# Optimization experiments

Hardware: AMD Instinct MI355X
Metric: run time of the kernel (lower is better)

## Reference

```python
import jax, jax.numpy as jnp
import numpy as np

B, S, F, H, T = 1024, 64, 2, 128, 24  # batch, src_len, n_features, hidden, output_length


def setup_inputs() -> dict:
    key = jax.random.key(0)
    ks = jax.random.split(key, 20)
    def p(k, shape):
        return jax.random.normal(k, shape, jnp.float32) * 0.05
    return {
        "x": jax.random.normal(ks[0], (B, S, F), jnp.float32),
        "prev_y": jnp.zeros((B, F), jnp.float32),
        # encoder 3-layer LSTM (PyTorch gate order i,f,g,o; b = b_ih + b_hh fused)
        "enc_Wih0": p(ks[1], (4 * H, F)),
        "enc_Whh0": p(ks[2], (4 * H, H)),
        "enc_b0": p(ks[3], (4 * H,)),
        "enc_Wih12": p(ks[4], (2, 4 * H, H)),
        "enc_Whh12": p(ks[5], (2, 4 * H, H)),
        "enc_b12": p(ks[6], (2, 4 * H)),
        # Bahdanau attention
        "attn_W": p(ks[7], (H, 2 * H)),
        "attn_b": p(ks[8], (H,)),
        "v_W": p(ks[9], (H,)),
        # decoder 3-layer LSTM, input size H+2
        "dec_Wih0": p(ks[10], (4 * H, H + 2)),
        "dec_Whh0": p(ks[11], (4 * H, H)),
        "dec_b0": p(ks[12], (4 * H,)),
        "dec_Wih12": p(ks[13], (2, 4 * H, H)),
        "dec_Whh12": p(ks[14], (2, 4 * H, H)),
        "dec_b12": p(ks[15], (2, 4 * H)),
        # output head Linear(2H, 2)
        "out_W": p(ks[16], (2, 2 * H)),
        "out_b": p(ks[17], (2,)),
    }


def _lstm_cell(xt, h, c, Wih, Whh, b):
    g = xt @ Wih.T + h @ Whh.T + b  # [B, 4H]
    i, f, gg, o = jnp.split(g, 4, axis=-1)
    c = jax.nn.sigmoid(f) * c + jax.nn.sigmoid(i) * jnp.tanh(gg)
    h = jax.nn.sigmoid(o) * jnp.tanh(c)
    return h, c


def _lstm_layer(xs, Wih, Whh, b):
    # xs: [S, B, in] -> hs [S, B, H], final (h, c)
    z = jnp.zeros((xs.shape[1], Whh.shape[1]), xs.dtype)
    def step(carry, xt):
        h, c = _lstm_cell(xt, carry[0], carry[1], Wih, Whh, b)
        return (h, c), h
    (hT, cT), hs = jax.lax.scan(step, (z, z), xs)
    return hs, hT, cT


def reference(x, prev_y, enc_Wih0, enc_Whh0, enc_b0, enc_Wih12, enc_Whh12, enc_b12,
              attn_W, attn_b, v_W, dec_Wih0, dec_Whh0, dec_b0, dec_Wih12, dec_Whh12,
              dec_b12, out_W, out_b):
    # ---- encoder: 3-layer LSTM over time ----
    hs, h0, c0 = _lstm_layer(jnp.swapaxes(x, 0, 1), enc_Wih0, enc_Whh0, enc_b0)
    hid, cel = [h0], [c0]
    for l in range(2):
        hs, hT, cT = _lstm_layer(hs, enc_Wih12[l], enc_Whh12[l], enc_b12[l])
        hid.append(hT); cel.append(cT)
    enc_out = jnp.swapaxes(hs, 0, 1)            # [B, S, H]
    h = jnp.stack(hid)                           # [3, B, H]
    c = jnp.stack(cel)

    def dec_step(carry, _):
        prev_out, h, c = carry
        h_top = h[2]                                             # top-layer hidden [B, H]
        a_in = jnp.concatenate(
            [jnp.broadcast_to(h_top[:, None, :], enc_out.shape), enc_out], axis=-1)  # [B, S, 2H]
        scores = jnp.tanh(a_in @ attn_W.T + attn_b) @ v_W        # [B, S]
        attw = jax.nn.softmax(scores, axis=1)
        weighted = jnp.einsum('bs,bsd->bd', attw, enc_out)        # [B, H]
        rnn_in = jnp.concatenate([prev_out, weighted], axis=-1)   # [B, H+2]
        h0n, c0n = _lstm_cell(rnn_in, h[0], c[0], dec_Wih0, dec_Whh0, dec_b0)
        h1n, c1n = _lstm_cell(h0n, h[1], c[1], dec_Wih12[0], dec_Whh12[0], dec_b12[0])
        h2n, c2n = _lstm_cell(h1n, h[2], c[2], dec_Wih12[1], dec_Whh12[1], dec_b12[1])
        out = jnp.concatenate([h2n, weighted], axis=-1) @ out_W.T + out_b  # [B, 2]
        return (out, jnp.stack([h0n, h1n, h2n]), jnp.stack([c0n, c1n, c2n])), out

    _, outs = jax.lax.scan(dec_step, (prev_y, h, c), None, length=T)
    return outs  # [T, B, 2]
```

## Files before the change

### kernel.cpp

```cpp
#include <hip/hip_runtime.h>
#include <hip/hip_fp16.h>

#define SEQ   64
#define HID   128
#define TOUT  24

typedef unsigned int u32;
typedef _Float16 f16;
typedef __attribute__((ext_vector_type(8))) f16 f16x8;
typedef __attribute__((ext_vector_type(4))) float f32x4;
#define MFMA __builtin_amdgcn_mfma_f32_16x16x32_f16

static __device__ __forceinline__ float sigm(float x){
  return __builtin_amdgcn_rcpf(1.f + __expf(-x));
}
static __device__ __forceinline__ float tanh_fast(float x){
  return fmaf(2.f, __builtin_amdgcn_rcpf(1.f + __expf(-2.f*x)), -1.f);
}

__global__ void prep_kernel(
    const float* __restrict__ eWih0,  const float* __restrict__ eWhh0,
    const float* __restrict__ eWih12, const float* __restrict__ eWhh12,
    const float* __restrict__ aW,
    const float* __restrict__ dWih0,  const float* __restrict__ dWhh0,
    const float* __restrict__ dWih12, const float* __restrict__ dWhh12,
    const float* __restrict__ oW,
    __half* __restrict__ wE0, __half* __restrict__ wE1, __half* __restrict__ wE2,
    __half* __restrict__ wD0, __half* __restrict__ wD1, __half* __restrict__ wD2,
    __half* __restrict__ wAh, __half* __restrict__ wAeF, float* __restrict__ wOT,
    float* __restrict__ dW2)
{
  int id = blockIdx.x*blockDim.x + threadIdx.x;
  if (id < 65536){
    int m=id, jj=m&7, l=(m>>3)&63, kt=(m>>9)&3, nt=m>>11;
    int col = nt*16 + (l&15), k = kt*32 + ((l>>4)<<3) + jj;
    wE0[m] = __float2half(eWhh0[col*128 + k]); return;
  }
  id -= 65536;
  if (id < 5*131072){
    int seg = id >> 17, m = id & 131071;
    int jj=m&7, l=(m>>3)&63, kt=(m>>9)&7, nt=m>>12;
    int col = nt*16 + (l&15), k = kt*32 + ((l>>4)<<3) + jj;
    float v;
    if (seg==0)      v = (k<128)? eWih12[col*128+k]         : eWhh12[col*128 + (k-128)];
    else if (seg==1) v = (k<128)? eWih12[65536+col*128+k]   : eWhh12[65536 + col*128 + (k-128)];
    else if (seg==2) v = (k<128)? dWih0[col*130 + 2 + k]    : dWhh0[col*128 + (k-128)];
    else if (seg==3) v = (k<128)? dWih12[col*128+k]         : dWhh12[col*128 + (k-128)];
    else             v = (k<128)? dWih12[65536+col*128+k]   : dWhh12[65536 + col*128 + (k-128)];
    __half* dst = (seg==0)?wE1:(seg==1)?wE2:(seg==2)?wD0:(seg==3)?wD1:wD2;
    dst[m] = __float2half(v); return;
  }
  id -= 5*131072;
  if (id < 16384){
    int m=id, jj=m&7, l=(m>>3)&63, kt=(m>>9)&3, nt=m>>11;
    int col = nt*16 + (l&15), k = kt*32 + ((l>>4)<<3) + jj;
    wAh[m] = __float2half(aW[col*256 + k]); return;
  }
  id -= 16384;
  if (id < 16384){
    int m=id, jj=m&7, l=(m>>3)&63, kt=(m>>9)&3, nt=m>>11;
    int col = nt*16 + (l&15), k = kt*32 + ((l>>4)<<3) + jj;
    wAeF[m] = __float2half(aW[col*256 + 128 + k]); return;
  }
  id -= 16384;
  if (id < 512){ int k=id>>1, jo=id&1; wOT[id] = oW[jo*256 + k]; return; }
  id -= 512;
  if (id < 1024){ int col=id>>1, ki=id&1; dW2[id] = dWih0[col*130 + ki]; return; }
}

__global__ __launch_bounds__(512) __attribute__((amdgpu_waves_per_eu(2, 2)))
void enc_kernel(
    const float* __restrict__ x, const float* __restrict__ eb0,
    const float* __restrict__ eb12, const float* __restrict__ eWih0,
    const __half* __restrict__ wE0, const __half* __restrict__ wE1,
    const __half* __restrict__ wE2,
    __half* __restrict__ hs0, __half* __restrict__ hs1,
    __half* __restrict__ carryH, float* __restrict__ carryC)
{
  __shared__ __align__(16) __half hT[2][2048];

  const int tid = threadIdx.x, w = tid>>6, lane = tid&63;
  const int l15 = lane&15, g4 = lane>>4;
  const int j = w*16 + l15;
  const int b16 = blockIdx.x*16;
  const int K0 = ((j>>5)*64 + ((j>>3)&3)*16)*8 + (j&7);

  __half* hs0b = hs0 + (size_t)blockIdx.x*131072;
  __half* hs1b = hs1 + (size_t)blockIdx.x*131072;

  for (int layer=0; layer<3; ++layer){
    const __half* W  = (layer==0)? wE0 : (layer==1)? wE1 : wE2;
    const float* bs  = (layer==0)? eb0 : (layer==1)? eb12 : (eb12+512);
    const __half* hinb  = (layer==1)? hs0b : hs1b;
    __half* houtb = (layer==0)? hs0b : (layer==1)? hs1b : nullptr;

    float bias[4];
#pragma unroll
    for (int g=0; g<4; ++g) bias[g] = bs[g*128 + j];
    float2 wx[4];
    if (layer==0){
#pragma unroll
      for (int g=0; g<4; ++g) wx[g] = *(const float2*)(eWih0 + (g*128+j)*2);
    }
    const f16x8* wb = (const f16x8*)W + lane;
    f16x8 Wh[16];
    if (layer==0){
#pragma unroll
      for (int g=0; g<4; ++g)
#pragma unroll
        for (int kt=0; kt<4; ++kt) Wh[g*4+kt] = wb[(size_t)((g*8+w)*4 + kt)*64];
    } else {
#pragma unroll
      for (int g=0; g<4; ++g)
#pragma unroll
        for (int kt=0; kt<4; ++kt) Wh[g*4+kt] = wb[(size_t)((g*8+w)*8 + 4 + kt)*64];
    }
    float c[4] = {0.f,0.f,0.f,0.f};
    ((u32*)hT[0])[tid] = 0u; ((u32*)hT[0])[tid+512] = 0u;
    __syncthreads();

    float2 xv[4]; f16x8 alo[4];
    if (layer==0){
#pragma unroll
      for (int q=0; q<4; ++q) xv[q] = *(const float2*)(x + ((size_t)(b16+g4*4+q)*SEQ + 0)*2);
    } else {
#pragma unroll
      for (int kt=0; kt<4; ++kt) alo[kt] = *(const f16x8*)(hinb + (kt*64+lane)*8);
    }

    int cur = 0;
    for (int t=0; t<SEQ; ++t){
      f16x8 wi[16];
      if (layer>0){
#pragma unroll
        for (int g=0; g<4; ++g)
#pragma unroll
          for (int kt=0; kt<4; ++kt) wi[g*4+kt] = wb[(size_t)((g*8+w)*8 + kt)*64];
      }
      f16x8 ah[4];
#pragma unroll
      for (int kt=0; kt<4; ++kt) ah[kt] = *(const f16x8*)(hT[cur] + (kt*64+lane)*8);
      float2 xcur[4]; f16x8 acur[4];
      if (layer==0){
#pragma unroll
        for (int q=0; q<4; ++q) xcur[q] = xv[q];
        if (t+1 < SEQ)
#pragma unroll
          for (int q=0; q<4; ++q) xv[q] = *(const float2*)(x + ((size_t)(b16+g4*4+q)*SEQ + t+1)*2);
      } else {
#pragma unroll
        for (int kt=0; kt<4; ++kt) acur[kt] = alo[kt];
        if (t+1 < SEQ)
#pragma unroll
          for (int kt=0; kt<4; ++kt) alo[kt] = *(const f16x8*)(hinb + (size_t)(t+1)*2048 + (kt*64+lane)*8);
      }
      f32x4 acc[4];
#pragma unroll
      for (int g=0; g<4; ++g) acc[g] = (f32x4){0.f,0.f,0.f,0.f};
#pragma unroll
      for (int g=0; g<4; ++g)
#pragma unroll
        for (int kt=0; kt<4; ++kt) acc[g] = MFMA(ah[kt], Wh[g*4+kt], acc[g], 0,0,0);
      if (layer>0){
#pragma unroll
        for (int g=0; g<4; ++g)
#pragma unroll
          for (int kt=0; kt<4; ++kt) acc[g] = MFMA(acur[kt], wi[g*4+kt], acc[g], 0,0,0);
      }
#pragma unroll
      for (int q=0; q<4; ++q){
        float gi = acc[0][q]+bias[0], gf = acc[1][q]+bias[1],
              gg = acc[2][q]+bias[2], go = acc[3][q]+bias[3];
        if (layer==0){
          gi += xcur[q].x*wx[0].x + xcur[q].y*wx[0].y;
          gf += xcur[q].x*wx[1].x + xcur[q].y*wx[1].y;
          gg += xcur[q].x*wx[2].x + xcur[q].y*wx[2].y;
          go += xcur[q].x*wx[3].x + xcur[q].y*wx[3].y;
        }
        float cn = fmaf(sigm(gf), c[q], sigm(gi)*tanh_fast(gg));
        float hn = sigm(go)*tanh_fast(cn);
        c[q] = cn;
        __half hh = __float2half(hn);
        hT[cur^1][K0 + (g4*4+q)*8] = hh;
        if (layer < 2){
          houtb[(size_t)t*2048 + K0 + (g4*4+q)*8] = hh;
        } else {
          int off = g4*32768 + q*8192 + (t>>4)*2048 + (j>>5)*512
                  + ((t&15) + ((j>>3)&3)*16)*8 + (j&7);
          hs0b[off] = hh;
        }
        if (t == SEQ-1){
          int ci = (layer*1024 + b16 + g4*4 + q)*128 + j;
          carryH[ci] = hh;
          carryC[ci] = cn;
        }
      }
      __syncthreads();
      cur ^= 1;
    }
    __syncthreads();
  }
}

#define LDQ(Q, g, kh) \
  Q[0] = wb[(size_t)((g)*64 + (kh)*4 + 0)*64]; \
  Q[1] = wb[(size_t)((g)*64 + (kh)*4 + 1)*64]; \
  Q[2] = wb[(size_t)((g)*64 + (kh)*4 + 2)*64]; \
  Q[3] = wb[(size_t)((g)*64 + (kh)*4 + 3)*64];
#define MM4(Q, A, g) \
  acc[g] = MFMA(A[0], Q[0], acc[g], 0,0,0); \
  acc[g] = MFMA(A[1], Q[1], acc[g], 0,0,0); \
  acc[g] = MFMA(A[2], Q[2], acc[g], 0,0,0); \
  acc[g] = MFMA(A[3], Q[3], acc[g], 0,0,0);

static __device__ __forceinline__ void dec_gemm(const __half* __restrict__ W,
    const __half* __restrict__ A0, const __half* __restrict__ A1,
    f32x4* acc, int lane, int w8)
{
  const f16x8* wb = (const f16x8*)W + (size_t)(w8*8)*64 + lane;
  f16x8 q0[4], q1[4], q2[4], q3[4];
  f16x8 a0[4], a1[4];
  LDQ(q0, 0, 0)
  LDQ(q1, 1, 0)
  LDQ(q2, 2, 0)
#pragma unroll
  for (int kt=0; kt<4; ++kt) a0[kt] = *(const f16x8*)(A0 + (kt*64+lane)*8);
#pragma unroll
  for (int g=0; g<4; ++g) acc[g] = (f32x4){0.f,0.f,0.f,0.f};
  MM4(q0, a0, 0)  LDQ(q3, 3, 0)
  MM4(q1, a0, 1)  LDQ(q0, 0, 1)
#pragma unroll
  for (int kt=0; kt<4; ++kt) a1[kt] = *(const f16x8*)(A1 + (kt*64+lane)*8);
  MM4(q2, a0, 2)  LDQ(q1, 1, 1)
  MM4(q3, a0, 3)  LDQ(q2, 2, 1)
  MM4(q0, a1, 0)  LDQ(q3, 3, 1)
  MM4(q1, a1, 1)
  MM4(q2, a1, 2)
  MM4(q3, a1, 3)
}

__global__ __launch_bounds__(512) __attribute__((amdgpu_waves_per_eu(2, 2)))
void dec_kernel(
    const float* __restrict__ prev_y, const float* __restrict__ db0,
    const float* __restrict__ db12, const float* __restrict__ ob,
    const float* __restrict__ ab, const float* __restrict__ vW,
    const __half* __restrict__ wD0, const __half* __restrict__ wD1,
    const __half* __restrict__ wD2, const __half* __restrict__ wAh,
    const __half* __restrict__ wAeF, const float* __restrict__ wOT,
    const float* __restrict__ dW2, const __half* __restrict__ encAg,
    const __half* __restrict__ carryH, const float* __restrict__ carryC,
    float* __restrict__ dout)
{
  __shared__ __align__(16) __half hT[4][2048];
  __shared__ float hp[4][132];
  __shared__ float scbF[256];
  __shared__ __align__(16) __half scb16h[256];
  __shared__ float hw[4*256];
  __shared__ float po[4][2];
  __shared__ float vwl[128];
  extern __shared__ __align__(16) __half dyn[];
  __half* encBL = dyn;
  __half* epL   = dyn + 32768;

  const int tid = threadIdx.x, w = tid>>6, lane = tid&63;
  const int l15 = lane&15, g4 = lane>>4;
  const int d = blockIdx.x, b4 = d*4;
  const int w8 = (w + d) & 7;
  const int j = w8*16 + l15;
  const int K0 = ((j>>5)*64 + ((j>>3)&3)*16)*8 + (j&7);
  const __half* encAd = encAg + (size_t)(d>>2)*131072 + (size_t)(d&3)*32768;

  float cD[3][4];
  if (g4 == 0){
#pragma unroll
    for (int l=0; l<3; ++l)
#pragma unroll
      for (int q=0; q<4; ++q){
        int ci = (l*1024 + b4 + q)*128 + j;
        hT[1+l][K0 + q*8] = carryH[ci];
        cD[l][q] = carryC[ci];
      }
  }
  if (tid < 8) po[tid>>1][tid&1] = prev_y[(b4 + (tid>>1))*2 + (tid&1)];
  if (tid < 128) vwl[tid] = vW[tid];

#pragma unroll
  for (int it=0; it<8; ++it){
    int lin = it*512 + tid;
    f16x8 v = *(const f16x8*)(encAd + (size_t)lin*8);
    int laneA = lin&63, ktA = (lin>>6)&3, sb = (lin>>8)&3, r4 = (lin>>10)&3;
    int s  = sb*16 + (laneA&15);
    int d0 = ktA*32 + ((laneA>>4)<<3);
    int base = r4*8192 + ((d0>>4)*2 + (s>>5))*512 + (s&7);
    int lb0  = (d0&15) + ((s>>3)&3)*16;
    f16* eb = (f16*)encBL;
#pragma unroll
    for (int u=0; u<8; ++u) eb[base + (lb0+u)*8] = v[u];
  }
#pragma unroll
  for (int i=0; i<2; ++i){
    int mt = w*2 + i, r4 = mt>>2, sb = mt&3;
    f16x8 a[4];
#pragma unroll
    for (int kt=0; kt<4; ++kt)
      a[kt] = *(const f16x8*)(encAd + (size_t)(((r4*4+sb)*4 + kt)*64 + lane)*8);
    const f16x8* bw = (const f16x8*)wAeF + lane;
#pragma unroll
    for (int nt=0; nt<8; ++nt){
      int col = nt*16 + l15;
      float abv = ab[col];
      f32x4 acc = {abv, abv, abv, abv};
#pragma unroll
      for (int kt=0; kt<4; ++kt) acc = MFMA(a[kt], bw[(size_t)(nt*4+kt)*64], acc, 0,0,0);
      int srow = r4*64 + sb*16 + g4*4;
#pragma unroll
      for (int q=0; q<4; ++q) epL[(srow+q)*132 + col] = __float2half(acc[q]);
    }
  }
  __syncthreads();

  auto cell = [&](float* crl, const float* bdp, const float* dwp, __half* hdst, float* hwp,
                  const f32x4* acc){
    float b0 = bdp[j], b1 = bdp[128+j], b2 = bdp[256+j], b3 = bdp[384+j];
    float2 w0, w1, w2, w3;
    if (dwp){
      w0 = *(const float2*)(dwp + 2*j);
      w1 = *(const float2*)(dwp + 2*(128+j));
      w2 = *(const float2*)(dwp + 2*(256+j));
      w3 = *(const float2*)(dwp + 2*(384+j));
    }
#pragma unroll
    for (int q=0; q<4; ++q){
      float gi = acc[0][q]+b0, gf = acc[1][q]+b1, gg = acc[2][q]+b2, go = acc[3][q]+b3;
      if (dwp){
        float p0 = po[q][0], p1 = po[q][1];
        gi += p0*w0.x + p1*w0.y;
        gf += p0*w1.x + p1*w1.y;
        gg += p0*w2.x + p1*w2.y;
        go += p0*w3.x + p1*w3.y;
      }
      float cn = fmaf(sigm(gf), crl[q], sigm(gi)*tanh_fast(gg));
      float hn = sigm(go)*tanh_fast(cn);
      crl[q] = cn;
      hdst[K0 + q*8] = __float2half(hn);
      if (hwp) hwp[q*256 + j] = hn;
    }
  };

  int zr = 0;
  for (int t=0; t<TOUT; ++t){
    asm volatile("" : "+v"(zr));
    const float*  db0t  = db0  + zr;
    const float*  db12t = db12 + zr;
    const float*  dW2t  = dW2  + zr;
    const __half* wAht  = wAh  + zr;

    {
      f16x8 a[4], wAhR[4];
      const f16x8* wbh = (const f16x8*)wAht + lane;
#pragma unroll
      for (int kt=0; kt<4; ++kt) wAhR[kt] = wbh[(size_t)(w8*4+kt)*64];
#pragma unroll
      for (int kt=0; kt<4; ++kt) a[kt] = *(const f16x8*)(hT[3] + (kt*64+lane)*8);
      f32x4 acc = {0.f,0.f,0.f,0.f};
#pragma unroll
      for (int kt=0; kt<4; ++kt) acc = MFMA(a[kt], wAhR[kt], acc, 0,0,0);
      if (g4 == 0){
#pragma unroll
        for (int q=0; q<4; ++q) hp[q][j] = acc[q];
      }
    }
    __syncthreads();
    {
      int rs = tid>>1, r = rs>>6, jh = tid&1;
      const __half* er = epL + rs*132 + jh*64;
      const float* hr = hp[r] + jh*64;
      const float* vr = vwl + jh*64;
      float sc = 0.f;
#pragma unroll
      for (int p=0; p<8; ++p){
        f16x8 e = *(const f16x8*)(er + p*8);
#pragma unroll
        for (int u=0; u<8; ++u)
          sc = fmaf(tanh_fast((float)e[u] + hr[p*8+u]), vr[p*8+u], sc);
      }
      sc += __shfl_xor(sc, 1);
      if (jh == 0) scbF[rs] = sc;
    }
    __syncthreads();
    if (tid < 256){
      float v = scbF[tid];
      float m = v;
#pragma unroll
      for (int off=32; off; off>>=1) m = fmaxf(m, __shfl_xor(m, off));
      float e = __expf(v - m);
      float sm = e;
#pragma unroll
      for (int off=32; off; off>>=1) sm += __shfl_xor(sm, off);
      scb16h[tid] = __float2half(e * __builtin_amdgcn_rcpf(sm));
    }
    __syncthreads();
    {
#pragma unroll
      for (int r=0; r<4; ++r){
        f32x4 acc = {0.f,0.f,0.f,0.f};
#pragma unroll
        for (int kt=0; kt<2; ++kt){
          f16x8 abc = *(const f16x8*)(scb16h + r*64 + kt*32 + ((lane>>4)<<3));
          f16x8 b   = *(const f16x8*)(encBL + r*8192 + ((w8*2+kt)*64 + lane)*8);
          acc = MFMA(abc, b, acc, 0,0,0);
        }
        if (lane < 16){
          hT[0][K0 + r*8] = __float2half(acc[0]);
          hw[r*256 + 128 + j] = acc[0];
        }
      }
    }
    __syncthreads();
    f32x4 acc[4];
    dec_gemm(wD0, hT[0], hT[1], acc, lane, w8);
    __syncthreads();
    if (g4 == 0) cell(cD[0], db0t, dW2t, hT[1], nullptr, acc);
    __syncthreads();
    dec_gemm(wD1, hT[1], hT[2], acc, lane, w8);
    __syncthreads();
    if (g4 == 0) cell(cD[1], db12t, nullptr, hT[2], nullptr, acc);
    __syncthreads();
    dec_gemm(wD2, hT[2], hT[3], acc, lane, w8);
    __syncthreads();
    if (g4 == 0) cell(cD[2], db12t + 512, nullptr, hT[3], hw, acc);
    __syncthreads();
    if (tid < 128){
      int r = tid>>5, kl = tid&31;
      float o0 = 0.f, o1 = 0.f;
#pragma unroll
      for (int i=0; i<8; ++i){
        int k = kl*8 + i;
        float hv = hw[r*256 + k];
        float2 wv = *(const float2*)(wOT + k*2);
        o0 = fmaf(hv, wv.x, o0); o1 = fmaf(hv, wv.y, o1);
      }
#pragma unroll
      for (int off=16; off; off>>=1){ o0 += __shfl_xor(o0, off); o1 += __shfl_xor(o1, off); }
      if (kl == 0){
        float v0 = o0 + ob[0], v1 = o1 + ob[1];
        size_t oi = ((size_t)t*1024 + b4 + r)*2;
        dout[oi] = v0; dout[oi+1] = v1;
        po[r][0] = v0; po[r][1] = v1;
      }
    }
    __syncthreads();
  }
}

extern "C" void kernel_launch(void* const* d_in, const int* in_sizes, int n_in,
                              void* d_out, int out_size, void* d_ws, size_t ws_size,
                              hipStream_t stream) {
  const float* x      = (const float*)d_in[0];
  const float* prev_y = (const float*)d_in[1];
  const float* eWih0  = (const float*)d_in[2];
  const float* eWhh0  = (const float*)d_in[3];
  const float* eb0    = (const float*)d_in[4];
  const float* eWih12 = (const float*)d_in[5];
  const float* eWhh12 = (const float*)d_in[6];
  const float* eb12   = (const float*)d_in[7];
  const float* aW     = (const float*)d_in[8];
  const float* ab     = (const float*)d_in[9];
  const float* vW     = (const float*)d_in[10];
  const float* dWih0  = (const float*)d_in[11];
  const float* dWhh0  = (const float*)d_in[12];
  const float* db0    = (const float*)d_in[13];
  const float* dWih12 = (const float*)d_in[14];
  const float* dWhh12 = (const float*)d_in[15];
  const float* db12   = (const float*)d_in[16];
  const float* oW     = (const float*)d_in[17];
  const float* ob     = (const float*)d_in[18];

  __half* wE0  = (__half*)d_ws;
  __half* wE1  = wE0 + 65536;
  __half* wE2  = wE1 + 131072;
  __half* wD0  = wE2 + 131072;
  __half* wD1  = wD0 + 131072;
  __half* wD2  = wD1 + 131072;
  __half* wAh  = wD2 + 131072;
  __half* wAeF = wAh + 16384;
  float*  wOT  = (float*)(wAeF + 16384);
  float*  dW2  = wOT + 512;
  __half* hs0  = (__half*)(dW2 + 1024);
  __half* hs1  = hs0 + (size_t)64*131072;
  __half* carryH = hs1 + (size_t)64*131072;
  float*  carryC = (float*)(carryH + 393216);

  const int prepN = 65536 + 5*131072 + 16384 + 16384 + 512 + 1024;
  prep_kernel<<<(prepN + 255)/256, 256, 0, stream>>>(
      eWih0, eWhh0, eWih12, eWhh12, aW, dWih0, dWhh0, dWih12, dWhh12, oW,
      wE0, wE1, wE2, wD0, wD1, wD2, wAh, wAeF, wOT, dW2);

  enc_kernel<<<64, 512, 0, stream>>>(
      x, eb0, eb12, eWih0, wE0, wE1, wE2, hs0, hs1, carryH, carryC);

  const int dynB = (32768 + 256*132) * 2;
  hipFuncSetAttribute(reinterpret_cast<const void*>(dec_kernel),
                      hipFuncAttributeMaxDynamicSharedMemorySize, dynB);
  dec_kernel<<<256, 512, dynB, stream>>>(
      prev_y, db0, db12, ob, ab, vW, wD0, wD1, wD2, wAh, wAeF, wOT, dW2,
      hs0, carryH, carryC, (float*)d_out);
}
```

Measured before the change: 624.2 us.

## Split decoder across 512 blocks of 2 batch rows and keep encoder values in registers

The decoder kernel now processes 2 batch rows per block instead of 4 and launches 512 blocks, so the serial 24-step recurrence is spread over more CUs. The shared-memory encoder copy is replaced by register-held MFMA B fragments, and the hw buffer is dropped: the output head reads h and the weighted context straight from the fp16 hT buffers. dec_gemm is also rewritten to double-buffer weight fragments with two register sets instead of four, cutting register pressure. Each block reloads the full decoder weights for half as many rows, so weight traffic per output doubles and half of every MFMA M tile is wasted.

```diff
diff --git a/kernel.cpp b/kernel.cpp
--- a/kernel.cpp
+++ b/kernel.cpp
@@ -218,25 +218,23 @@
     f32x4* acc, int lane, int w8)
 {
   const f16x8* wb = (const f16x8*)W + (size_t)(w8*8)*64 + lane;
-  f16x8 q0[4], q1[4], q2[4], q3[4];
-  f16x8 a0[4], a1[4];
-  LDQ(q0, 0, 0)
-  LDQ(q1, 1, 0)
-  LDQ(q2, 2, 0)
+  f16x8 qA[4], qB[4], a0[4], a1[4];
+  LDQ(qA, 0, 0)
+  LDQ(qB, 1, 0)
 #pragma unroll
   for (int kt=0; kt<4; ++kt) a0[kt] = *(const f16x8*)(A0 + (kt*64+lane)*8);
 #pragma unroll
   for (int g=0; g<4; ++g) acc[g] = (f32x4){0.f,0.f,0.f,0.f};
-  MM4(q0, a0, 0)  LDQ(q3, 3, 0)
-  MM4(q1, a0, 1)  LDQ(q0, 0, 1)
+  MM4(qA, a0, 0)  LDQ(qA, 2, 0)
+  MM4(qB, a0, 1)  LDQ(qB, 3, 0)
 #pragma unroll
   for (int kt=0; kt<4; ++kt) a1[kt] = *(const f16x8*)(A1 + (kt*64+lane)*8);
-  MM4(q2, a0, 2)  LDQ(q1, 1, 1)
-  MM4(q3, a0, 3)  LDQ(q2, 2, 1)
-  MM4(q0, a1, 0)  LDQ(q3, 3, 1)
-  MM4(q1, a1, 1)
-  MM4(q2, a1, 2)
-  MM4(q3, a1, 3)
+  MM4(qA, a0, 2)  LDQ(qA, 0, 1)
+  MM4(qB, a0, 3)  LDQ(qB, 1, 1)
+  MM4(qA, a1, 0)  LDQ(qA, 2, 1)
+  MM4(qB, a1, 1)  LDQ(qB, 3, 1)
+  MM4(qA, a1, 2)
+  MM4(qB, a1, 3)
 }
 
 __global__ __launch_bounds__(512) __attribute__((amdgpu_waves_per_eu(2, 2)))
@@ -252,58 +250,57 @@
     float* __restrict__ dout)
 {
   __shared__ __align__(16) __half hT[4][2048];
-  __shared__ float hp[4][132];
-  __shared__ float scbF[256];
-  __shared__ __align__(16) __half scb16h[256];
-  __shared__ float hw[4*256];
-  __shared__ float po[4][2];
+  __shared__ float hp[2][132];
+  __shared__ float scbF[128];
+  __shared__ __align__(16) __half scb16h[128];
+  __shared__ float po[2][2];
   __shared__ float vwl[128];
   extern __shared__ __align__(16) __half dyn[];
-  __half* encBL = dyn;
-  __half* epL   = dyn + 32768;
+  __half* epL = dyn;
 
   const int tid = threadIdx.x, w = tid>>6, lane = tid&63;
   const int l15 = lane&15, g4 = lane>>4;
-  const int d = blockIdx.x, b4 = d*4;
+  const int d = blockIdx.x, b2 = d*2;
   const int w8 = (w + d) & 7;
   const int j = w8*16 + l15;
   const int K0 = ((j>>5)*64 + ((j>>3)&3)*16)*8 + (j&7);
-  const __half* encAd = encAg + (size_t)(d>>2)*131072 + (size_t)(d&3)*32768;
-
-  float cD[3][4];
+  const __half* encR0 = encAg + (size_t)(b2>>4)*131072
+                      + (size_t)((b2&15)>>2)*32768 + (size_t)(b2&3)*8192;
+
+  float cD[3][2];
   if (g4 == 0){
 #pragma unroll
     for (int l=0; l<3; ++l)
 #pragma unroll
-      for (int q=0; q<4; ++q){
-        int ci = (l*1024 + b4 + q)*128 + j;
+      for (int q=0; q<2; ++q){
+        int ci = (l*1024 + b2 + q)*128 + j;
         hT[1+l][K0 + q*8] = carryH[ci];
         cD[l][q] = carryC[ci];
       }
   }
-  if (tid < 8) po[tid>>1][tid&1] = prev_y[(b4 + (tid>>1))*2 + (tid&1)];
+  if (tid < 4) po[tid>>1][tid&1] = prev_y[(b2 + (tid>>1))*2 + (tid&1)];
   if (tid < 128) vwl[tid] = vW[tid];
 
-#pragma unroll
-  for (int it=0; it<8; ++it){
-    int lin = it*512 + tid;
-    f16x8 v = *(const f16x8*)(encAd + (size_t)lin*8);
-    int laneA = lin&63, ktA = (lin>>6)&3, sb = (lin>>8)&3, r4 = (lin>>10)&3;
-    int s  = sb*16 + (laneA&15);
-    int d0 = ktA*32 + ((laneA>>4)<<3);
-    int base = r4*8192 + ((d0>>4)*2 + (s>>5))*512 + (s&7);
-    int lb0  = (d0&15) + ((s>>3)&3)*16;
-    f16* eb = (f16*)encBL;
-#pragma unroll
-    for (int u=0; u<8; ++u) eb[base + (lb0+u)*8] = v[u];
-  }
-#pragma unroll
-  for (int i=0; i<2; ++i){
-    int mt = w*2 + i, r4 = mt>>2, sb = mt&3;
+  f16x8 eBr[2][2];
+#pragma unroll
+  for (int rr=0; rr<2; ++rr)
+#pragma unroll
+    for (int kt=0; kt<2; ++kt){
+      int bs = kt*32 + g4*8;
+      const __half* src = encR0 + rr*8192 + (bs>>4)*2048 + (j>>5)*512
+                        + ((bs&15) + ((j>>3)&3)*16)*8 + (j&7);
+      f16x8 v;
+#pragma unroll
+      for (int u=0; u<8; ++u) v[u] = (f16)src[(size_t)u*8];
+      eBr[rr][kt] = v;
+    }
+
+  {
+    int rr = w>>2, sb = w&3;
+    const __half* arow = encR0 + rr*8192 + sb*2048;
     f16x8 a[4];
 #pragma unroll
-    for (int kt=0; kt<4; ++kt)
-      a[kt] = *(const f16x8*)(encAd + (size_t)(((r4*4+sb)*4 + kt)*64 + lane)*8);
+    for (int kt=0; kt<4; ++kt) a[kt] = *(const f16x8*)(arow + (kt*64+lane)*8);
     const f16x8* bw = (const f16x8*)wAeF + lane;
 #pragma unroll
     for (int nt=0; nt<8; ++nt){
@@ -312,16 +309,16 @@
       f32x4 acc = {abv, abv, abv, abv};
 #pragma unroll
       for (int kt=0; kt<4; ++kt) acc = MFMA(a[kt], bw[(size_t)(nt*4+kt)*64], acc, 0,0,0);
-      int srow = r4*64 + sb*16 + g4*4;
+      int srow = rr*64 + sb*16 + g4*4;
 #pragma unroll
       for (int q=0; q<4; ++q) epL[(srow+q)*132 + col] = __float2half(acc[q]);
     }
   }
   __syncthreads();
 
-  auto cell = [&](float* crl, const float* bdp, const float* dwp, __half* hdst, float* hwp,
+  auto cell = [&](float* crl, const float* bdp, const float* dwp, __half* hdst,
                   const f32x4* acc){
-    float b0 = bdp[j], b1 = bdp[128+j], b2 = bdp[256+j], b3 = bdp[384+j];
+    float b0 = bdp[j], b1 = bdp[128+j], b2_ = bdp[256+j], b3 = bdp[384+j];
     float2 w0, w1, w2, w3;
     if (dwp){
       w0 = *(const float2*)(dwp + 2*j);
@@ -330,8 +327,8 @@
       w3 = *(const float2*)(dwp + 2*(384+j));
     }
 #pragma unroll
-    for (int q=0; q<4; ++q){
-      float gi = acc[0][q]+b0, gf = acc[1][q]+b1, gg = acc[2][q]+b2, go = acc[3][q]+b3;
+    for (int q=0; q<2; ++q){
+      float gi = acc[0][q]+b0, gf = acc[1][q]+b1, gg = acc[2][q]+b2_, go = acc[3][q]+b3;
       if (dwp){
         float p0 = po[q][0], p1 = po[q][1];
         gi += p0*w0.x + p1*w0.y;
@@ -343,7 +340,6 @@
       float hn = sigm(go)*tanh_fast(cn);
       crl[q] = cn;
       hdst[K0 + q*8] = __float2half(hn);
-      if (hwp) hwp[q*256 + j] = hn;
     }
   };
 
@@ -366,29 +362,30 @@
 #pragma unroll
       for (int kt=0; kt<4; ++kt) acc = MFMA(a[kt], wAhR[kt], acc, 0,0,0);
       if (g4 == 0){
-#pragma unroll
-        for (int q=0; q<4; ++q) hp[q][j] = acc[q];
+        hp[0][j] = acc[0];
+        hp[1][j] = acc[1];
       }
     }
     __syncthreads();
     {
-      int rs = tid>>1, r = rs>>6, jh = tid&1;
-      const __half* er = epL + rs*132 + jh*64;
-      const float* hr = hp[r] + jh*64;
-      const float* vr = vwl + jh*64;
+      int rs = tid>>2, jq = tid&3, r = rs>>6;
+      const __half* er = epL + rs*132 + jq*32;
+      const float* hr = hp[r] + jq*32;
+      const float* vr = vwl + jq*32;
       float sc = 0.f;
 #pragma unroll
-      for (int p=0; p<8; ++p){
+      for (int p=0; p<4; ++p){
         f16x8 e = *(const f16x8*)(er + p*8);
 #pragma unroll
         for (int u=0; u<8; ++u)
           sc = fmaf(tanh_fast((float)e[u] + hr[p*8+u]), vr[p*8+u], sc);
       }
       sc += __shfl_xor(sc, 1);
-      if (jh == 0) scbF[rs] = sc;
-    }
-    __syncthreads();
-    if (tid < 256){
+      sc += __shfl_xor(sc, 2);
+      if (jq == 0) scbF[rs] = sc;
+    }
+    __syncthreads();
+    if (tid < 128){
       float v = scbF[tid];
       float m = v;
 #pragma unroll
@@ -402,49 +399,47 @@
     __syncthreads();
     {
 #pragma unroll
-      for (int r=0; r<4; ++r){
+      for (int rr=0; rr<2; ++rr){
         f32x4 acc = {0.f,0.f,0.f,0.f};
 #pragma unroll
         for (int kt=0; kt<2; ++kt){
-          f16x8 abc = *(const f16x8*)(scb16h + r*64 + kt*32 + ((lane>>4)<<3));
-          f16x8 b   = *(const f16x8*)(encBL + r*8192 + ((w8*2+kt)*64 + lane)*8);
-          acc = MFMA(abc, b, acc, 0,0,0);
+          f16x8 abc = *(const f16x8*)(scb16h + rr*64 + kt*32 + g4*8);
+          acc = MFMA(abc, eBr[rr][kt], acc, 0,0,0);
         }
-        if (lane < 16){
-          hT[0][K0 + r*8] = __float2half(acc[0]);
-          hw[r*256 + 128 + j] = acc[0];
-        }
+        if (lane < 16) hT[0][K0 + rr*8] = __float2half(acc[0]);
       }
     }
     __syncthreads();
     f32x4 acc[4];
     dec_gemm(wD0, hT[0], hT[1], acc, lane, w8);
     __syncthreads();
-    if (g4 == 0) cell(cD[0], db0t, dW2t, hT[1], nullptr, acc);
+    if (g4 == 0) cell(cD[0], db0t, dW2t, hT[1], acc);
     __syncthreads();
     dec_gemm(wD1, hT[1], hT[2], acc, lane, w8);
     __syncthreads();
-    if (g4 == 0) cell(cD[1], db12t, nullptr, hT[2], nullptr, acc);
+    if (g4 == 0) cell(cD[1], db12t, nullptr, hT[2], acc);
     __syncthreads();
     dec_gemm(wD2, hT[2], hT[3], acc, lane, w8);
     __syncthreads();
-    if (g4 == 0) cell(cD[2], db12t + 512, nullptr, hT[3], hw, acc);
+    if (g4 == 0) cell(cD[2], db12t + 512, nullptr, hT[3], acc);
     __syncthreads();
     if (tid < 128){
-      int r = tid>>5, kl = tid&31;
-      float o0 = 0.f, o1 = 0.f;
-#pragma unroll
-      for (int i=0; i<8; ++i){
-        int k = kl*8 + i;
-        float hv = hw[r*256 + k];
-        float2 wv = *(const float2*)(wOT + k*2);
-        o0 = fmaf(hv, wv.x, o0); o1 = fmaf(hv, wv.y, o1);
-      }
-#pragma unroll
-      for (int off=16; off; off>>=1){ o0 += __shfl_xor(o0, off); o1 += __shfl_xor(o1, off); }
+      int r = tid>>6, kl = tid&63;
+      int k2 = kl*2;
+      int sl = ((k2>>5)*64 + r + ((k2>>3)&3)*16)*8 + (k2&7);
+      float2 h2f = __half22float2(*(const __half2*)(hT[3] + sl));
+      float2 wwf = __half22float2(*(const __half2*)(hT[0] + sl));
+      float2 a0 = *(const float2*)(wOT + k2*2);
+      float2 a1 = *(const float2*)(wOT + k2*2 + 2);
+      float2 b0v = *(const float2*)(wOT + (128+k2)*2);
+      float2 b1v = *(const float2*)(wOT + (128+k2)*2 + 2);
+      float o0 = h2f.x*a0.x + h2f.y*a1.x + wwf.x*b0v.x + wwf.y*b1v.x;
+      float o1 = h2f.x*a0.y + h2f.y*a1.y + wwf.x*b0v.y + wwf.y*b1v.y;
+#pragma unroll
+      for (int off=32; off; off>>=1){ o0 += __shfl_xor(o0, off); o1 += __shfl_xor(o1, off); }
       if (kl == 0){
         float v0 = o0 + ob[0], v1 = o1 + ob[1];
-        size_t oi = ((size_t)t*1024 + b4 + r)*2;
+        size_t oi = ((size_t)t*1024 + b2 + r)*2;
         dout[oi] = v0; dout[oi+1] = v1;
         po[r][0] = v0; po[r][1] = v1;
       }
@@ -499,10 +494,10 @@
   enc_kernel<<<64, 512, 0, stream>>>(
       x, eb0, eb12, eWih0, wE0, wE1, wE2, hs0, hs1, carryH, carryC);
 
-  const int dynB = (32768 + 256*132) * 2;
+  const int dynB = 128*132*2;
   hipFuncSetAttribute(reinterpret_cast<const void*>(dec_kernel),
                       hipFuncAttributeMaxDynamicSharedMemorySize, dynB);
-  dec_kernel<<<256, 512, dynB, stream>>>(
+  dec_kernel<<<512, 512, dynB, stream>>>(
       prev_y, db0, db12, ob, ab, vW, wD0, wD1, wD2, wAh, wAeF, wOT, dW2,
       hs0, carryH, carryC, (float*)d_out);
 }
```

Result: slower. 882.1 us (+41.3%).
